# Optimization experiments

Hardware: AMD Instinct MI355X
Metric: run time of the kernel (lower is better)

The kernel has to match this reference:

```python
import jax, jax.numpy as jnp
import numpy as np
import math

HEAD_DIM = 64

def setup_inputs() -> dict:
    key = jax.random.key(0)
    k1, k2, k3, k4 = jax.random.split(key, 4)
    B, T, E, H = 4096, 128, 256, HEAD_DIM
    x = jax.random.normal(k1, (B, T, E), dtype=jnp.float32)
    # torch nn.Linear init scale ~ U(-1/sqrt(E), 1/sqrt(E)); use scaled normal for simplicity
    s = 1.0 / math.sqrt(E)
    Wq = jax.random.normal(k2, (E, H), dtype=jnp.float32) * s
    Wk = jax.random.normal(k3, (E, H), dtype=jnp.float32) * s
    Wv = jax.random.normal(k4, (E, H), dtype=jnp.float32) * s
    return {"x": x, "Wq": Wq, "Wk": Wk, "Wv": Wv}

def reference(x, Wq, Wk, Wv):
    # x: [B, T, E]; Wq/Wk/Wv: [E, H]
    T = x.shape[1]
    H = Wq.shape[1]
    Q = jnp.einsum('bte,eh->bth', x, Wq)
    K = jnp.einsum('bte,eh->bth', x, Wk)
    V = jnp.einsum('bte,eh->bth', x, Wv)
    scores = jnp.einsum('bqh,bkh->bqk', Q, K) / jnp.sqrt(jnp.float32(H))  # [B,T,T]
    causal = jnp.tril(jnp.ones((T, T), dtype=bool))
    scores = jnp.where(causal, scores, -jnp.inf)
    weights = jax.nn.softmax(scores, axis=-1)
    # dropout omitted (eval mode / deterministic reference)
    out = jnp.einsum('bqk,bkh->bqh', weights, V)  # [B,T,H]
    return out
```

## Files before the change

### kernel.cpp

```cpp
#include <hip/hip_runtime.h>

#define NB 4096
#define TT 128
#define EE 256
#define HH 64

typedef __attribute__((ext_vector_type(8))) short bf16x8;
typedef __attribute__((ext_vector_type(4))) float f32x4;
typedef __attribute__((ext_vector_type(2))) unsigned int u32x2;

#define QK_STRIDE 72
#define P_STRIDE  136
#define VT_STRIDE 136

__device__ __forceinline__ unsigned short f2bf(float f) {
  union { float f; unsigned u; } c; c.f = f;
  return (unsigned short)((c.u + 0x7fffu + ((c.u >> 16) & 1u)) >> 16);
}

__device__ __forceinline__ unsigned cvt_pk(float lo, float hi) {
  unsigned r;
  asm("v_cvt_pk_bf16_f32 %0, %1, %2" : "=v"(r) : "v"(lo), "v"(hi));
  return r;
}

__device__ __forceinline__ bf16x8 cvt8(f32x4 a, f32x4 b) {
  union { unsigned u[4]; bf16x8 v; } r;
  r.u[0] = cvt_pk(a[0], a[1]);
  r.u[1] = cvt_pk(a[2], a[3]);
  r.u[2] = cvt_pk(b[0], b[1]);
  r.u[3] = cvt_pk(b[2], b[3]);
  return r.v;
}

__global__ void prep_w(const float* __restrict__ wq, const float* __restrict__ wk,
                       const float* __restrict__ wv, unsigned short* __restrict__ wt) {
  __shared__ float tile[64][65];
  const int wi = blockIdx.x >> 2;
  const int et = blockIdx.x & 3;
  const float* __restrict__ w = (wi == 0) ? wq : (wi == 1) ? wk : wv;
  const int tx = threadIdx.x & 63;
  const int ty = threadIdx.x >> 6;
#pragma unroll
  for (int it = 0; it < 16; ++it) {
    int el = ty + 4 * it;
    tile[el][tx] = w[(et * 64 + el) * HH + tx];
  }
  __syncthreads();
#pragma unroll
  for (int it = 0; it < 16; ++it) {
    int nl = ty + 4 * it;
    wt[(wi * 64 + nl) * EE + et * 64 + tx] = f2bf(tile[tx][nl]);
  }
}

template <int NTB>
__device__ __forceinline__ void qkv_pass(const float* __restrict__ xb,
                                         const unsigned short* __restrict__ wt,
                                         unsigned short* qbuf, unsigned short* kbuf,
                                         unsigned short* sVT,
                                         int r0, int r1, int l16, int quad) {
  const int rb[2] = {r0, r1};
  f32x4 acc[6][2];
#pragma unroll
  for (int j = 0; j < 6; ++j)
#pragma unroll
    for (int mt = 0; mt < 2; ++mt)
      acc[j][mt] = (f32x4){0.f, 0.f, 0.f, 0.f};

  f32x4 xf[2][2][2];
#pragma unroll
  for (int p = 0; p < 2; ++p)
#pragma unroll
    for (int mt = 0; mt < 2; ++mt) {
      const float* s = xb + (rb[mt] + l16) * EE + p * 32 + quad * 8;
      xf[p][mt][0] = *(const f32x4*)s;
      xf[p][mt][1] = *(const f32x4*)(s + 4);
    }

  bf16x8 bcur[6];
#pragma unroll
  for (int j = 0; j < 6; ++j)
    bcur[j] = *(const bf16x8*)(wt + ((NTB + j) * 16 + l16) * EE + quad * 8);

#pragma unroll
  for (int kc = 0; kc < 8; ++kc) {
    const int pb = kc & 1;
    bf16x8 afr[2];
    afr[0] = cvt8(xf[pb][0][0], xf[pb][0][1]);
    afr[1] = cvt8(xf[pb][1][0], xf[pb][1][1]);
    if (kc < 6) {
#pragma unroll
      for (int mt = 0; mt < 2; ++mt) {
        const float* s = xb + (rb[mt] + l16) * EE + (kc + 2) * 32 + quad * 8;
        xf[pb][mt][0] = *(const f32x4*)s;
        xf[pb][mt][1] = *(const f32x4*)(s + 4);
      }
    }
    bf16x8 bnext[6];
    if (kc < 7) {
#pragma unroll
      for (int j = 0; j < 6; ++j)
        bnext[j] = *(const bf16x8*)(wt + ((NTB + j) * 16 + l16) * EE + (kc + 1) * 32 + quad * 8);
    }
    __builtin_amdgcn_s_setprio(1);
#pragma unroll
    for (int j = 0; j < 6; ++j) {
      acc[j][0] = __builtin_amdgcn_mfma_f32_16x16x32_bf16(afr[0], bcur[j], acc[j][0], 0, 0, 0);
      acc[j][1] = __builtin_amdgcn_mfma_f32_16x16x32_bf16(afr[1], bcur[j], acc[j][1], 0, 0, 0);
    }
    __builtin_amdgcn_s_setprio(0);
#pragma unroll
    for (int j = 0; j < 6; ++j) bcur[j] = bnext[j];
  }

#pragma unroll
  for (int j = 0; j < 6; ++j) {
    const int nt = NTB + j;
    const int cg = nt * 16 + l16;
#pragma unroll
    for (int mt = 0; mt < 2; ++mt) {
      const int rbase = rb[mt] + 4 * quad;
      unsigned p01 = cvt_pk(acc[j][mt][0], acc[j][mt][1]);
      unsigned p23 = cvt_pk(acc[j][mt][2], acc[j][mt][3]);
      if (nt < 8) {
        unsigned short* dst = (nt < 4) ? (qbuf + rbase * QK_STRIDE + cg)
                                       : (kbuf + rbase * QK_STRIDE + (cg - 64));
        dst[0]             = (unsigned short)p01;
        dst[QK_STRIDE]     = (unsigned short)(p01 >> 16);
        dst[2 * QK_STRIDE] = (unsigned short)p23;
        dst[3 * QK_STRIDE] = (unsigned short)(p23 >> 16);
      } else {
        u32x2 pv = {p01, p23};
        *(u32x2*)(sVT + (cg - 128) * VT_STRIDE + rbase) = pv;
      }
    }
  }
}

__global__ __launch_bounds__(256, 3)
void attn_fused(const float* __restrict__ x, const unsigned short* __restrict__ wt,
                float* __restrict__ out) {
  __shared__ __align__(16) unsigned short sQK[2 * TT * QK_STRIDE];
  __shared__ __align__(16) unsigned short sVT[HH * VT_STRIDE];
  unsigned short* qbuf = sQK;
  unsigned short* kbuf = sQK + TT * QK_STRIDE;
  unsigned short* pbuf = sQK;

  const int b    = blockIdx.x;
  const int tid  = threadIdx.x;
  const int w    = tid >> 6;
  const int lane = tid & 63;
  const int quad = lane >> 4;
  const int l16  = lane & 15;

  const int t0 = w, t1 = 7 - w;
  const int rb[2]  = {16 * t0, 16 * t1};
  const int ntn[2] = {t0 + 1, t1 + 1};

  const float* __restrict__ xb = x + (size_t)b * TT * EE;

  qkv_pass<0>(xb, wt, qbuf, kbuf, sVT, rb[0], rb[1], l16, quad);
  qkv_pass<6>(xb, wt, qbuf, kbuf, sVT, rb[0], rb[1], l16, quad);
  __syncthreads();

  f32x4 sacc[2][8];
#pragma unroll
  for (int i = 0; i < 2; ++i)
#pragma unroll
    for (int nt = 0; nt < 8; ++nt)
      sacc[i][nt] = (f32x4){0.f, 0.f, 0.f, 0.f};

#pragma unroll
  for (int kk = 0; kk < 2; ++kk) {
#pragma unroll
    for (int i = 0; i < 2; ++i) {
      bf16x8 aq = *(const bf16x8*)(qbuf + (rb[i] + l16) * QK_STRIDE + kk * 32 + quad * 8);
      __builtin_amdgcn_s_setprio(1);
#pragma unroll
      for (int nt = 0; nt < 8; ++nt) {
        if (nt < ntn[i]) {
          bf16x8 bk = *(const bf16x8*)(kbuf + (nt * 16 + l16) * QK_STRIDE + kk * 32 + quad * 8);
          sacc[i][nt] = __builtin_amdgcn_mfma_f32_16x16x32_bf16(aq, bk, sacc[i][nt], 0, 0, 0);
        }
      }
      __builtin_amdgcn_s_setprio(0);
    }
  }
  __syncthreads();

  const float scale = 0.125f;
#pragma unroll
  for (int i = 0; i < 2; ++i) {
    const int ntnW = ntn[i];
    const int ntnPad = (ntnW + 1) & ~1;
#pragma unroll
    for (int r = 0; r < 4; ++r) {
      int row = rb[i] + 4 * quad + r;
      float mx = -3.0e38f;
#pragma unroll
      for (int nt = 0; nt < 8; ++nt) {
        if (nt < ntnW) {
          int c = nt * 16 + l16;
          float s = (c <= row) ? sacc[i][nt][r] * scale : -3.0e38f;
          sacc[i][nt][r] = s;
          mx = fmaxf(mx, s);
        }
      }
#pragma unroll
      for (int off = 1; off < 16; off <<= 1) mx = fmaxf(mx, __shfl_xor(mx, off, 64));
      float sum = 0.f;
#pragma unroll
      for (int nt = 0; nt < 8; ++nt) {
        if (nt < ntnW) {
          float e = __expf(sacc[i][nt][r] - mx);
          sacc[i][nt][r] = e;
          sum += e;
        }
      }
#pragma unroll
      for (int off = 1; off < 16; off <<= 1) sum += __shfl_xor(sum, off, 64);
      float inv = 1.0f / sum;
#pragma unroll
      for (int np = 0; np < 4; ++np) {
        if (2 * np < ntnPad) {
          float v0 = (2 * np     < ntnW) ? sacc[i][2 * np][r] * inv     : 0.f;
          float v1 = (2 * np + 1 < ntnW) ? sacc[i][2 * np + 1][r] * inv : 0.f;
          unsigned p = cvt_pk(v0, v1);
          pbuf[row * P_STRIDE + (2 * np) * 16 + l16]     = (unsigned short)p;
          pbuf[row * P_STRIDE + (2 * np + 1) * 16 + l16] = (unsigned short)(p >> 16);
        }
      }
    }
  }

  f32x4 oacc[2][4];
#pragma unroll
  for (int i = 0; i < 2; ++i)
#pragma unroll
    for (int nt = 0; nt < 4; ++nt)
      oacc[i][nt] = (f32x4){0.f, 0.f, 0.f, 0.f};

  const int ksn[2] = {t0 / 2 + 1, t1 / 2 + 1};
#pragma unroll
  for (int i = 0; i < 2; ++i) {
#pragma unroll
    for (int ks = 0; ks < 4; ++ks) {
      if (ks < ksn[i]) {
        bf16x8 ap = *(const bf16x8*)(pbuf + (rb[i] + l16) * P_STRIDE + ks * 32 + quad * 8);
        __builtin_amdgcn_s_setprio(1);
#pragma unroll
        for (int nt = 0; nt < 4; ++nt) {
          bf16x8 bv = *(const bf16x8*)(sVT + (nt * 16 + l16) * VT_STRIDE + ks * 32 + quad * 8);
          oacc[i][nt] = __builtin_amdgcn_mfma_f32_16x16x32_bf16(ap, bv, oacc[i][nt], 0, 0, 0);
        }
        __builtin_amdgcn_s_setprio(0);
      }
    }
  }

  float* __restrict__ ob = out + (size_t)b * TT * HH;
#pragma unroll
  for (int i = 0; i < 2; ++i) {
#pragma unroll
    for (int r = 0; r < 4; ++r) {
      int row = rb[i] + 4 * quad + r;
#pragma unroll
      for (int nt = 0; nt < 4; ++nt)
        ob[row * HH + nt * 16 + l16] = oacc[i][nt][r];
    }
  }
}

extern "C" void kernel_launch(void* const* d_in, const int* in_sizes, int n_in,
                              void* d_out, int out_size, void* d_ws, size_t ws_size,
                              hipStream_t stream) {
  const float* x  = (const float*)d_in[0];
  const float* wq = (const float*)d_in[1];
  const float* wk = (const float*)d_in[2];
  const float* wv = (const float*)d_in[3];
  unsigned short* wt = (unsigned short*)d_ws;
  float* outp = (float*)d_out;

  prep_w<<<dim3(12), dim3(256), 0, stream>>>(wq, wk, wv, wt);
  attn_fused<<<dim3(NB), dim3(256), 0, stream>>>(x, wt, outp);
}
```

Baseline: 888.3 us.

## Load x once into bf16 registers and split QKV projection into three passes

Before, each of the two QKV passes streamed x from global memory and converted it to bf16 again. Now x is loaded once, converted into a register-resident bf16 fragment array (16 bf16x8 per lane) through a 4-deep load ring, and reused across three projection passes of 4 output tiles each (Q, K, V). This halves the global reads of x and removes the repeated conversions. In exchange the kernel holds 64 extra VGPRs per lane for the cached fragments, which may cause spills or lower occupancy under the 3-blocks-per-CU launch bound.

```diff
diff --git a/kernel.cpp b/kernel.cpp
--- a/kernel.cpp
+++ b/kernel.cpp
@@ -55,84 +55,65 @@
 }
 
 template <int NTB>
-__device__ __forceinline__ void qkv_pass(const float* __restrict__ xb,
-                                         const unsigned short* __restrict__ wt,
-                                         unsigned short* qbuf, unsigned short* kbuf,
-                                         unsigned short* sVT,
-                                         int r0, int r1, int l16, int quad) {
+__device__ __forceinline__ void qkv_pass4(const bf16x8 xr[2][8],
+                                          const unsigned short* __restrict__ wt,
+                                          unsigned short* qbuf, unsigned short* kbuf,
+                                          unsigned short* sVT,
+                                          int r0, int r1, int l16, int quad) {
   const int rb[2] = {r0, r1};
-  f32x4 acc[6][2];
-#pragma unroll
-  for (int j = 0; j < 6; ++j)
+  f32x4 acc[4][2];
+#pragma unroll
+  for (int j = 0; j < 4; ++j)
 #pragma unroll
     for (int mt = 0; mt < 2; ++mt)
       acc[j][mt] = (f32x4){0.f, 0.f, 0.f, 0.f};
 
-  f32x4 xf[2][2][2];
-#pragma unroll
-  for (int p = 0; p < 2; ++p)
-#pragma unroll
-    for (int mt = 0; mt < 2; ++mt) {
-      const float* s = xb + (rb[mt] + l16) * EE + p * 32 + quad * 8;
-      xf[p][mt][0] = *(const f32x4*)s;
-      xf[p][mt][1] = *(const f32x4*)(s + 4);
-    }
-
-  bf16x8 bcur[6];
-#pragma unroll
-  for (int j = 0; j < 6; ++j)
+  bf16x8 bcur[4];
+#pragma unroll
+  for (int j = 0; j < 4; ++j)
     bcur[j] = *(const bf16x8*)(wt + ((NTB + j) * 16 + l16) * EE + quad * 8);
 
 #pragma unroll
   for (int kc = 0; kc < 8; ++kc) {
-    const int pb = kc & 1;
-    bf16x8 afr[2];
-    afr[0] = cvt8(xf[pb][0][0], xf[pb][0][1]);
-    afr[1] = cvt8(xf[pb][1][0], xf[pb][1][1]);
-    if (kc < 6) {
-#pragma unroll
-      for (int mt = 0; mt < 2; ++mt) {
-        const float* s = xb + (rb[mt] + l16) * EE + (kc + 2) * 32 + quad * 8;
-        xf[pb][mt][0] = *(const f32x4*)s;
-        xf[pb][mt][1] = *(const f32x4*)(s + 4);
-      }
-    }
-    bf16x8 bnext[6];
+    bf16x8 bnext[4];
     if (kc < 7) {
 #pragma unroll
-      for (int j = 0; j < 6; ++j)
+      for (int j = 0; j < 4; ++j)
         bnext[j] = *(const bf16x8*)(wt + ((NTB + j) * 16 + l16) * EE + (kc + 1) * 32 + quad * 8);
     }
     __builtin_amdgcn_s_setprio(1);
 #pragma unroll
-    for (int j = 0; j < 6; ++j) {
-      acc[j][0] = __builtin_amdgcn_mfma_f32_16x16x32_bf16(afr[0], bcur[j], acc[j][0], 0, 0, 0);
-      acc[j][1] = __builtin_amdgcn_mfma_f32_16x16x32_bf16(afr[1], bcur[j], acc[j][1], 0, 0, 0);
+    for (int j = 0; j < 4; ++j) {
+      acc[j][0] = __builtin_amdgcn_mfma_f32_16x16x32_bf16(xr[0][kc], bcur[j], acc[j][0], 0, 0, 0);
+      acc[j][1] = __builtin_amdgcn_mfma_f32_16x16x32_bf16(xr[1][kc], bcur[j], acc[j][1], 0, 0, 0);
     }
     __builtin_amdgcn_s_setprio(0);
 #pragma unroll
-    for (int j = 0; j < 6; ++j) bcur[j] = bnext[j];
-  }
-
-#pragma unroll
-  for (int j = 0; j < 6; ++j) {
-    const int nt = NTB + j;
-    const int cg = nt * 16 + l16;
+    for (int j = 0; j < 4; ++j) bcur[j] = bnext[j];
+  }
+
+#pragma unroll
+  for (int j = 0; j < 4; ++j) {
 #pragma unroll
     for (int mt = 0; mt < 2; ++mt) {
       const int rbase = rb[mt] + 4 * quad;
       unsigned p01 = cvt_pk(acc[j][mt][0], acc[j][mt][1]);
       unsigned p23 = cvt_pk(acc[j][mt][2], acc[j][mt][3]);
-      if (nt < 8) {
-        unsigned short* dst = (nt < 4) ? (qbuf + rbase * QK_STRIDE + cg)
-                                       : (kbuf + rbase * QK_STRIDE + (cg - 64));
+      if (NTB == 0) {
+        unsigned short* dst = qbuf + rbase * QK_STRIDE + j * 16 + l16;
+        dst[0]             = (unsigned short)p01;
+        dst[QK_STRIDE]     = (unsigned short)(p01 >> 16);
+        dst[2 * QK_STRIDE] = (unsigned short)p23;
+        dst[3 * QK_STRIDE] = (unsigned short)(p23 >> 16);
+      } else if (NTB == 4) {
+        unsigned short* dst = kbuf + rbase * QK_STRIDE + j * 16 + l16;
         dst[0]             = (unsigned short)p01;
         dst[QK_STRIDE]     = (unsigned short)(p01 >> 16);
         dst[2 * QK_STRIDE] = (unsigned short)p23;
         dst[3 * QK_STRIDE] = (unsigned short)(p23 >> 16);
       } else {
         u32x2 pv = {p01, p23};
-        *(u32x2*)(sVT + (cg - 128) * VT_STRIDE + rbase) = pv;
+        *(u32x2*)(sVT + (j * 16 + l16) * VT_STRIDE + rbase) = pv;
       }
     }
   }
@@ -160,8 +141,32 @@
 
   const float* __restrict__ xb = x + (size_t)b * TT * EE;
 
-  qkv_pass<0>(xb, wt, qbuf, kbuf, sVT, rb[0], rb[1], l16, quad);
-  qkv_pass<6>(xb, wt, qbuf, kbuf, sVT, rb[0], rb[1], l16, quad);
+  bf16x8 xr[2][8];
+  {
+    f32x4 land[4][2];
+#pragma unroll
+    for (int c = 0; c < 4; ++c) {
+      const int kc = c >> 1, mt = c & 1;
+      const float* s = xb + (rb[mt] + l16) * EE + kc * 32 + quad * 8;
+      land[c][0] = *(const f32x4*)s;
+      land[c][1] = *(const f32x4*)(s + 4);
+    }
+#pragma unroll
+    for (int c = 0; c < 16; ++c) {
+      const int kc = c >> 1, mt = c & 1;
+      xr[mt][kc] = cvt8(land[c & 3][0], land[c & 3][1]);
+      if (c + 4 < 16) {
+        const int cn = c + 4, kcn = cn >> 1, mtn = cn & 1;
+        const float* s = xb + (rb[mtn] + l16) * EE + kcn * 32 + quad * 8;
+        land[c & 3][0] = *(const f32x4*)s;
+        land[c & 3][1] = *(const f32x4*)(s + 4);
+      }
+    }
+  }
+
+  qkv_pass4<0>(xr, wt, qbuf, kbuf, sVT, rb[0], rb[1], l16, quad);
+  qkv_pass4<4>(xr, wt, qbuf, kbuf, sVT, rb[0], rb[1], l16, quad);
+  qkv_pass4<8>(xr, wt, qbuf, kbuf, sVT, rb[0], rb[1], l16, quad);
   __syncthreads();
 
   f32x4 sacc[2][8];
```

After: 907.4 us. 1.02x slower.
